# Optimization experiments

Hardware: AMD Instinct MI355X
Metric: run time of the kernel (lower is better)

Reference implementation:

```python
import jax, jax.numpy as jnp
import numpy as np

D, H, DFF, MD = 1024, 16, 4096, 128
B, TS, TT = 8, 512, 512
EPS = 1e-6


def _ln(x, s, b):
    m = jnp.mean(x, axis=-1, keepdims=True)
    v = jnp.mean((x - m) ** 2, axis=-1, keepdims=True)
    return (x - m) * jax.lax.rsqrt(v + EPS) * s + b


def _rel_bias(emb, qlen, klen):
    # T5-style bidirectional bucket: [H, qlen, klen]
    q = jnp.arange(qlen)[:, None]
    k = jnp.arange(klen)[None, :]
    rp = k - q
    bucket = jnp.where(rp < 0, jnp.minimum(-rp, MD - 1), jnp.minimum(rp, MD - 1) + MD)
    return emb[bucket].transpose(2, 0, 1)


def _mha(xq, xkv, w_in, b_in, w_out, b_out, bias):
    # nn.MultiheadAttention math: packed in_proj [3D,D], additive attn bias [H,Tq,Tk]
    Bq, Tq, _ = xq.shape
    Tk = xkv.shape[1]
    hd = D // H
    wq, wk, wv = jnp.split(w_in, 3, axis=0)
    bq, bk, bv = jnp.split(b_in, 3, axis=0)
    q = (xq @ wq.T + bq).reshape(Bq, Tq, H, hd).transpose(0, 2, 1, 3)
    k = (xkv @ wk.T + bk).reshape(Bq, Tk, H, hd).transpose(0, 2, 1, 3)
    v = (xkv @ wv.T + bv).reshape(Bq, Tk, H, hd).transpose(0, 2, 1, 3)
    scores = jnp.einsum('bhqd,bhkd->bhqk', q, k) / jnp.sqrt(jnp.asarray(hd, xq.dtype))
    scores = scores + bias[None]
    attn = jax.nn.softmax(scores, axis=-1)
    out = jnp.einsum('bhqk,bhkd->bhqd', attn, v)
    out = out.transpose(0, 2, 1, 3).reshape(Bq, Tq, D)
    return out @ w_out.T + b_out


def setup_inputs() -> dict:
    key = jax.random.key(0)
    ks = jax.random.split(key, 40)
    std = 0.02

    def n(i, shape):
        return jax.random.normal(ks[i], shape, dtype=jnp.float32) * std

    return {
        'src': jax.random.normal(ks[0], (B, TS, D), dtype=jnp.float32),
        'tgt': jax.random.normal(ks[1], (B, TT, D), dtype=jnp.float32),
        # encoder layer
        'enc_in_w': n(2, (3 * D, D)), 'enc_in_b': jnp.zeros((3 * D,)),
        'enc_out_w': n(3, (D, D)), 'enc_out_b': jnp.zeros((D,)),
        'enc_ff1_w': n(4, (DFF, D)), 'enc_ff1_b': jnp.zeros((DFF,)),
        'enc_ff2_w': n(5, (D, DFF)), 'enc_ff2_b': jnp.zeros((D,)),
        'enc_n1_s': jnp.ones((D,)), 'enc_n1_b': jnp.zeros((D,)),
        'enc_n2_s': jnp.ones((D,)), 'enc_n2_b': jnp.zeros((D,)),
        'enc_rel': n(6, (2 * MD, H)),
        # decoder layer
        'dec_sa_in_w': n(7, (3 * D, D)), 'dec_sa_in_b': jnp.zeros((3 * D,)),
        'dec_sa_out_w': n(8, (D, D)), 'dec_sa_out_b': jnp.zeros((D,)),
        'dec_ca_in_w': n(9, (3 * D, D)), 'dec_ca_in_b': jnp.zeros((3 * D,)),
        'dec_ca_out_w': n(10, (D, D)), 'dec_ca_out_b': jnp.zeros((D,)),
        'dec_ff1_w': n(11, (DFF, D)), 'dec_ff1_b': jnp.zeros((DFF,)),
        'dec_ff2_w': n(12, (D, DFF)), 'dec_ff2_b': jnp.zeros((D,)),
        'dec_n1_s': jnp.ones((D,)), 'dec_n1_b': jnp.zeros((D,)),
        'dec_n2_s': jnp.ones((D,)), 'dec_n2_b': jnp.zeros((D,)),
        'dec_n3_s': jnp.ones((D,)), 'dec_n3_b': jnp.zeros((D,)),
        'dec_rel_self': n(13, (2 * MD, H)),
        'dec_rel_cross': n(14, (2 * MD, H)),
    }


def reference(src, tgt,
              enc_in_w, enc_in_b, enc_out_w, enc_out_b,
              enc_ff1_w, enc_ff1_b, enc_ff2_w, enc_ff2_b,
              enc_n1_s, enc_n1_b, enc_n2_s, enc_n2_b, enc_rel,
              dec_sa_in_w, dec_sa_in_b, dec_sa_out_w, dec_sa_out_b,
              dec_ca_in_w, dec_ca_in_b, dec_ca_out_w, dec_ca_out_b,
              dec_ff1_w, dec_ff1_b, dec_ff2_w, dec_ff2_b,
              dec_n1_s, dec_n1_b, dec_n2_s, dec_n2_b, dec_n3_s, dec_n3_b,
              dec_rel_self, dec_rel_cross):
    Ts, Tt = src.shape[1], tgt.shape[1]

    # ---- encoder layer (pre-LN) ----
    eb = _rel_bias(enc_rel, Ts, Ts)  # [H,Ts,Ts]
    x = src
    x = x + _mha(_ln(x, enc_n1_s, enc_n1_b), _ln(x, enc_n1_s, enc_n1_b),
                 enc_in_w, enc_in_b, enc_out_w, enc_out_b, eb)
    h = _ln(x, enc_n2_s, enc_n2_b)
    x = x + (jax.nn.relu(h @ enc_ff1_w.T + enc_ff1_b) @ enc_ff2_w.T + enc_ff2_b)
    memory = x

    # ---- decoder layer (pre-LN) ----
    causal = jnp.where(jnp.arange(Tt)[None, :] > jnp.arange(Tt)[:, None], -jnp.inf, 0.0)
    sb = _rel_bias(dec_rel_self, Tt, Tt) + causal[None]  # [H,Tt,Tt]
    cb = _rel_bias(dec_rel_cross, Tt, Ts)                # [H,Tt,Ts]
    y = tgt
    yn = _ln(y, dec_n1_s, dec_n1_b)
    y = y + _mha(yn, yn, dec_sa_in_w, dec_sa_in_b, dec_sa_out_w, dec_sa_out_b, sb)
    y = y + _mha(_ln(y, dec_n2_s, dec_n2_b), memory,
                 dec_ca_in_w, dec_ca_in_b, dec_ca_out_w, dec_ca_out_b, cb)
    h = _ln(y, dec_n3_s, dec_n3_b)
    y = y + (jax.nn.relu(h @ dec_ff1_w.T + dec_ff1_b) @ dec_ff2_w.T + dec_ff2_b)
    return y
```

## Files before the change

kernel.cpp:

```cpp
#include <hip/hip_runtime.h>

using u16 = unsigned short;

typedef float f32x4 __attribute__((ext_vector_type(4)));
typedef __bf16 bf16x8v __attribute__((ext_vector_type(8)));
typedef bf16x8v bf16x8 __attribute__((may_alias));
typedef u16 u16x8v __attribute__((ext_vector_type(8)));
typedef u16x8v u16x8 __attribute__((may_alias));
typedef u16 u16x4v __attribute__((ext_vector_type(4)));
typedef u16x4v u16x4 __attribute__((may_alias));
typedef float f32x4v __attribute__((ext_vector_type(4)));
typedef f32x4v float4a __attribute__((may_alias));

#define GPTR(p) ((__attribute__((address_space(1))) void*)(p))
#define LPTR(p) ((__attribute__((address_space(3))) void*)(p))

__device__ __forceinline__ u16 f2bf(float f) {
  unsigned u = __builtin_bit_cast(unsigned, f);
  u += 0x7FFFu + ((u >> 16) & 1u);
  return (u16)(u >> 16);
}

__device__ __forceinline__ f32x4 mfma16(bf16x8 a, bf16x8 b, f32x4 c) {
  return __builtin_amdgcn_mfma_f32_16x16x32_bf16(a, b, c, 0, 0, 0);
}

struct Srcs { const float* s[10]; };

__global__ __launch_bounds__(256) void cvt_all(Srcs srcs, u16* __restrict__ dst) {
  constexpr int off[11] = {0, 786432, 1048576, 2097152, 3145728,
                           3932160, 4194304, 4980736, 5242880, 6291456, 7340032};
  const int i = blockIdx.x * 256 + threadIdx.x;
  int r = 0;
#pragma unroll
  for (int j = 1; j < 10; j++) r += (i >= off[j]);
  float4a v = ((const float4a*)srcs.s[r])[i - off[r]];
  u16x4 o;
  o[0] = f2bf(v[0]); o[1] = f2bf(v[1]); o[2] = f2bf(v[2]); o[3] = f2bf(v[3]);
  ((u16x4*)dst)[i] = o;
}

__global__ __launch_bounds__(256) void add_cvt(const float* __restrict__ a,
                                               const float* __restrict__ b,
                                               u16* __restrict__ o) {
  const int i = blockIdx.x * 256 + threadIdx.x;
  float4a va = ((const float4a*)a)[i];
  float4a vb = ((const float4a*)b)[i];
  u16x4 ov;
#pragma unroll
  for (int j = 0; j < 4; j++) ov[j] = f2bf(va[j] + vb[j]);
  ((u16x4*)o)[i] = ov;
}

__global__ __launch_bounds__(256) void add_f32(float* __restrict__ o,
                                               const float* __restrict__ b) {
  const int i = blockIdx.x * 256 + threadIdx.x;
  float4a vo = ((float4a*)o)[i];
  float4a vb = ((const float4a*)b)[i];
#pragma unroll
  for (int j = 0; j < 4; j++) vo[j] += vb[j];
  ((float4a*)o)[i] = vo;
}

__global__ __launch_bounds__(256) void ln_k(const float* __restrict__ x,
                                            const float* __restrict__ sc,
                                            const float* __restrict__ bi,
                                            u16* __restrict__ out) {
  const int row = blockIdx.x, tid = threadIdx.x;
  float4a v = ((const float4a*)(x + (size_t)row * 1024))[tid];
  float s1 = v[0] + v[1] + v[2] + v[3];
  float s2 = v[0]*v[0] + v[1]*v[1] + v[2]*v[2] + v[3]*v[3];
#pragma unroll
  for (int off = 32; off; off >>= 1) { s1 += __shfl_xor(s1, off); s2 += __shfl_xor(s2, off); }
  __shared__ float red[8];
  if ((tid & 63) == 0) { red[tid >> 6] = s1; red[4 + (tid >> 6)] = s2; }
  __syncthreads();
  s1 = red[0] + red[1] + red[2] + red[3];
  s2 = red[4] + red[5] + red[6] + red[7];
  const float mean = s1 * (1.f / 1024.f);
  const float rstd = rsqrtf(s2 * (1.f / 1024.f) - mean * mean + 1e-6f);
  float4a s4 = ((const float4a*)sc)[tid];
  float4a b4 = ((const float4a*)bi)[tid];
  u16x4 o;
#pragma unroll
  for (int j = 0; j < 4; j++) o[j] = f2bf((v[j] - mean) * rstd * s4[j] + b4[j]);
  ((u16x4*)(out + (size_t)row * 1024))[tid] = o;
}

template <int BN_T, int MW, int EPI, int PF>
__global__ __launch_bounds__(256) void gemm_bt(
    const u16* __restrict__ A, int lda,
    const u16* __restrict__ W, int ldw,
    const float* __restrict__ bias,
    const float* __restrict__ C0, int ldc0,
    void* __restrict__ outv, int ldo, int K,
    float* __restrict__ part) {
  constexpr int BM = 128, BK = 64;
  constexpr int NW = 4 / MW;
  constexpr int FM = BM / MW / 16;
  constexpr int FN = BN_T / NW / 16;
  constexpr int RA = (BM * BK * 2) / 4096;
  constexpr int RB = (BN_T * BK * 2) / 4096;
  constexpr int NB = PF ? 2 : 1;
  __shared__ alignas(16) u16 As[NB][BM * BK];
  __shared__ alignas(16) u16 Bs[NB][BN_T * BK];
  const int tid = threadIdx.x, lane = tid & 63, wv = tid >> 6;
  const int kb = (EPI == 3) ? blockIdx.z * K : 0;

  const int gx = gridDim.x;
  const int nwg = gx * gridDim.y;
  const int orig = blockIdx.y * gx + blockIdx.x;
  const int qq = nwg >> 3, rr = nwg & 7;
  const int xcd = orig & 7, idx = orig >> 3;
  const int wg = (xcd < rr ? xcd * (qq + 1) : rr * (qq + 1) + (xcd - rr) * qq) + idx;
  const int bm = (wg / gx) * BM, bn = (wg % gx) * BN_T;

  const int wr = (wv / NW) * (BM / MW);
  const int wc = (wv % NW) * (BN_T / NW);
  const int la = lane & 15, lg = lane >> 4;
  const int r7 = la & 7;
  const int srow = wv * 8 + (lane >> 3);
  const int scol = ((lane & 7) ^ (lane >> 3)) << 3;
  const u16* gA = A + (size_t)(bm + srow) * lda + scol;
  const u16* gB = W + (size_t)(bn + srow) * ldw + scol;

  f32x4 acc[FM][FN] = {};

  auto stage = [&](int buf, int k0) {
#pragma unroll
    for (int r = 0; r < RA; r++)
      __builtin_amdgcn_global_load_lds(GPTR(gA + (size_t)r * 32 * lda + k0),
                                       LPTR(&As[buf][(wv * 8 + r * 32) * BK]), 16, 0, 0);
#pragma unroll
    for (int r = 0; r < RB; r++)
      __builtin_amdgcn_global_load_lds(GPTR(gB + (size_t)r * 32 * ldw + k0),
                                       LPTR(&Bs[buf][(wv * 8 + r * 32) * BK]), 16, 0, 0);
  };

  auto compute = [&](int buf) {
#pragma unroll
    for (int kk = 0; kk < BK; kk += 32) {
      const int off = ((((kk >> 3) + lg) ^ r7) << 3);
      bf16x8 af[FM], bfr[FN];
#pragma unroll
      for (int m = 0; m < FM; m++)
        af[m] = *(const bf16x8*)&As[buf][(wr + m * 16 + la) * BK + off];
#pragma unroll
      for (int n = 0; n < FN; n++)
        bfr[n] = *(const bf16x8*)&Bs[buf][(wc + n * 16 + la) * BK + off];
#pragma unroll
      for (int m = 0; m < FM; m++)
#pragma unroll
        for (int n = 0; n < FN; n++)
          acc[m][n] = mfma16(af[m], bfr[n], acc[m][n]);
    }
  };

  if constexpr (PF) {
    stage(0, kb);
    int buf = 0;
    const int NT = K / BK;
    for (int t = 0; t < NT; ++t) {
      if (t + 1 < NT) {
        stage(buf ^ 1, kb + (t + 1) * BK);
        if constexpr (RA + RB == 8)
          asm volatile("s_waitcnt vmcnt(8)" ::: "memory");
        else
          asm volatile("s_waitcnt vmcnt(6)" ::: "memory");
      } else {
        asm volatile("s_waitcnt vmcnt(0)" ::: "memory");
      }
      __builtin_amdgcn_s_barrier();
      __builtin_amdgcn_sched_barrier(0);
      compute(buf);
      __builtin_amdgcn_s_barrier();
      buf ^= 1;
    }
  } else {
    for (int k0 = 0; k0 < K; k0 += BK) {
      __syncthreads();
      stage(0, kb + k0);
      __syncthreads();
      compute(0);
    }
  }

  const bool addb = (EPI != 3) || (blockIdx.z == 0);
  float bv[FN];
#pragma unroll
  for (int n = 0; n < FN; n++) bv[n] = addb ? bias[bn + wc + n * 16 + la] : 0.f;
#pragma unroll
  for (int m = 0; m < FM; m++) {
#pragma unroll
    for (int j = 0; j < 4; j++) {
      const int row = bm + wr + m * 16 + (lane >> 4) * 4 + j;
#pragma unroll
      for (int n = 0; n < FN; n++) {
        const int col = bn + wc + n * 16 + la;
        float v = acc[m][n][j] + bv[n];
        if constexpr (EPI == 1) v = fmaxf(v, 0.f);
        if constexpr (EPI == 2) {
          ((float*)outv)[(size_t)row * ldo + col] = v + C0[(size_t)row * ldc0 + col];
        } else if constexpr (EPI == 3) {
          if (blockIdx.z == 0)
            ((float*)outv)[(size_t)row * ldo + col] = v + C0[(size_t)row * ldc0 + col];
          else
            part[(size_t)row * ldo + col] = v;
        } else {
          ((u16*)outv)[(size_t)row * ldo + col] = f2bf(v);
        }
      }
    }
  }
}

template <bool CAUSAL>
__global__ __launch_bounds__(256) void attn_k(
    const u16* __restrict__ Qb, int ldq,
    const u16* __restrict__ Kb, int ldk,
    const u16* __restrict__ Vb, int ldv,
    const float* __restrict__ rel,
    u16* __restrict__ Ob, int ldo,
    int Tq, int Tk) {
  __shared__ alignas(16) u16 Ks[128][72];
  __shared__ alignas(16) u16 Vt[64][136];
  __shared__ alignas(16) u16 Ps[4][16][136];
  __shared__ float biasl[256];
  const int tid = threadIdx.x, lane = tid & 63, w = tid >> 6;
  const int b = blockIdx.y >> 4, h = blockIdx.y & 15;
  const int q0 = blockIdx.x * 64;
  const int la = lane & 15, lg = lane >> 4;

  biasl[tid] = rel[tid * 16 + h];

  const int qr0 = q0 + w * 16;
  const u16* qp = Qb + (size_t)(b * Tq + qr0 + la) * ldq + h * 64 + lg * 8;
  const bf16x8 qf0 = *(const bf16x8*)qp;
  const bf16x8 qf1 = *(const bf16x8*)(qp + 32);

  float m[4], sm[4];
  f32x4 acc[4] = {};
#pragma unroll
  for (int j = 0; j < 4; j++) { m[j] = -1e30f; sm[j] = 0.f; }

  const int kv_end = CAUSAL ? (q0 + 64) : Tk;
  const int srow = tid >> 3, scol = (tid & 7) * 8;
  for (int kv0 = 0; kv0 < kv_end; kv0 += 128) {
    __syncthreads();
#pragma unroll
    for (int r = 0; r < 4; r++) {
      const int row = r * 32 + srow;
      const size_t gr = (size_t)(b * Tk + kv0 + row);
      *(u16x8*)&Ks[row][scol] = *(const u16x8*)&Kb[gr * ldk + h * 64 + scol];
      u16x8 vv = *(const u16x8*)&Vb[gr * ldv + h * 64 + scol];
#pragma unroll
      for (int j = 0; j < 8; j++) Vt[scol + j][row] = vv[j];
    }
    __syncthreads();

    f32x4 s[8];
#pragma unroll
    for (int kvt = 0; kvt < 8; kvt++) {
      const bf16x8 kf0 = *(const bf16x8*)&Ks[kvt * 16 + la][lg * 8];
      const bf16x8 kf1 = *(const bf16x8*)&Ks[kvt * 16 + la][32 + lg * 8];
      f32x4 t = {};
      t = mfma16(qf0, kf0, t);
      t = mfma16(qf1, kf1, t);
      const int kc = kv0 + kvt * 16 + la;
#pragma unroll
      for (int j = 0; j < 4; j++) {
        const int qr = qr0 + lg * 4 + j;
        const int rp = kc - qr;
        const int bucket = rp < 0 ? (rp > -127 ? -rp : 127) : (rp < 127 ? rp : 127) + 128;
        float sv = t[j] * 0.125f + biasl[bucket];
        if (CAUSAL && kc > qr) sv = -1e30f;
        s[kvt][j] = sv;
      }
    }
    float alpha[4];
#pragma unroll
    for (int j = 0; j < 4; j++) {
      float tm = s[0][j];
#pragma unroll
      for (int kvt = 1; kvt < 8; kvt++) tm = fmaxf(tm, s[kvt][j]);
#pragma unroll
      for (int off = 1; off < 16; off <<= 1) tm = fmaxf(tm, __shfl_xor(tm, off));
      const float mn = fmaxf(m[j], tm);
      alpha[j] = __expf(m[j] - mn);
      m[j] = mn;
      float r = 0.f;
#pragma unroll
      for (int kvt = 0; kvt < 8; kvt++) {
        const float p = __expf(s[kvt][j] - mn);
        s[kvt][j] = p;
        r += p;
      }
#pragma unroll
      for (int off = 1; off < 16; off <<= 1) r += __shfl_xor(r, off);
      sm[j] = sm[j] * alpha[j] + r;
    }
#pragma unroll
    for (int kvt = 0; kvt < 8; kvt++)
#pragma unroll
      for (int j = 0; j < 4; j++)
        Ps[w][lg * 4 + j][kvt * 16 + la] = f2bf(s[kvt][j]);
#pragma unroll
    for (int n = 0; n < 4; n++)
#pragma unroll
      for (int j = 0; j < 4; j++)
        acc[n][j] *= alpha[j];
#pragma unroll
    for (int kq = 0; kq < 4; kq++) {
      const bf16x8 pf = *(const bf16x8*)&Ps[w][la][kq * 32 + lg * 8];
#pragma unroll
      for (int n = 0; n < 4; n++) {
        const bf16x8 vf = *(const bf16x8*)&Vt[n * 16 + la][kq * 32 + lg * 8];
        acc[n] = mfma16(pf, vf, acc[n]);
      }
    }
  }
#pragma unroll
  for (int n = 0; n < 4; n++)
#pragma unroll
    for (int j = 0; j < 4; j++) {
      const int qr = qr0 + lg * 4 + j;
      Ob[(size_t)(b * Tq + qr) * ldo + h * 64 + n * 16 + la] = f2bf(acc[n][j] / sm[j]);
    }
}

extern "C" void kernel_launch(void* const* d_in, const int* in_sizes, int n_in,
                              void* d_out, int out_size, void* d_ws, size_t ws_size,
                              hipStream_t stream) {
  (void)in_sizes; (void)n_in; (void)out_size; (void)ws_size;
  const float* src       = (const float*)d_in[0];
  const float* tgt       = (const float*)d_in[1];
  const float* enc_in_w  = (const float*)d_in[2];
  const float* enc_in_b  = (const float*)d_in[3];
  const float* enc_out_w = (const float*)d_in[4];
  const float* enc_out_b = (const float*)d_in[5];
  const float* enc_ff1_w = (const float*)d_in[6];
  const float* enc_ff1_b = (const float*)d_in[7];
  const float* enc_ff2_w = (const float*)d_in[8];
  const float* enc_ff2_b = (const float*)d_in[9];
  const float* enc_n1_s  = (const float*)d_in[10];
  const float* enc_n1_b  = (const float*)d_in[11];
  const float* enc_n2_s  = (const float*)d_in[12];
  const float* enc_n2_b  = (const float*)d_in[13];
  const float* enc_rel   = (const float*)d_in[14];
  const float* dsa_in_w  = (const float*)d_in[15];
  const float* dsa_in_b  = (const float*)d_in[16];
  const float* dsa_out_w = (const float*)d_in[17];
  const float* dsa_out_b = (const float*)d_in[18];
  const float* dca_in_w  = (const float*)d_in[19];
  const float* dca_in_b  = (const float*)d_in[20];
  const float* dca_out_w = (const float*)d_in[21];
  const float* dca_out_b = (const float*)d_in[22];
  const float* dff1_w    = (const float*)d_in[23];
  const float* dff1_b    = (const float*)d_in[24];
  const float* dff2_w    = (const float*)d_in[25];
  const float* dff2_b    = (const float*)d_in[26];
  const float* dn1_s     = (const float*)d_in[27];
  const float* dn1_b     = (const float*)d_in[28];
  const float* dn2_s     = (const float*)d_in[29];
  const float* dn2_b     = (const float*)d_in[30];
  const float* dn3_s     = (const float*)d_in[31];
  const float* dn3_b     = (const float*)d_in[32];
  const float* drel_s    = (const float*)d_in[33];
  const float* drel_c    = (const float*)d_in[34];
  float* fo = (float*)d_out;

  char* w8 = (char*)d_ws;
  float* x_ws  = (float*)(w8 + 0);
  u16* ln_buf  = (u16*)(w8 + 16777216);
  u16* qkv     = (u16*)(w8 + 25165824);
  u16* attn_o  = (u16*)(w8 + 50331648);
  u16* ffh     = qkv;
  u16* memb    = (u16*)(w8 + 58720256);
  u16* wb      = (u16*)(w8 + 67108864);

  u16* w_enc_in  = wb;
  u16* w_enc_out = wb + 3145728;
  u16* w_enc_f1  = wb + 4194304;
  u16* w_enc_f2  = wb + 8388608;
  u16* w_dsa_in  = wb + 12582912;
  u16* w_dsa_out = wb + 15728640;
  u16* w_dca_in  = wb + 16777216;
  u16* w_dca_out = wb + 19922944;
  u16* w_dff1    = wb + 20971520;
  u16* w_dff2    = wb + 25165824;

  Srcs srcs = {{enc_in_w, enc_out_w, enc_ff1_w, enc_ff2_w, dsa_in_w,
                dsa_out_w, dca_in_w, dca_out_w, dff1_w, dff2_w}};
  cvt_all<<<dim3(28672), 256, 0, stream>>>(srcs, wb);

  ln_k<<<dim3(4096), 256, 0, stream>>>(src, enc_n1_s, enc_n1_b, ln_buf);
  gemm_bt<128,2,0,0><<<dim3(24, 32), 256, 0, stream>>>(ln_buf, 1024, w_enc_in, 1024, enc_in_b, nullptr, 0, qkv, 3072, 1024, nullptr);
  attn_k<false><<<dim3(8, 128), 256, 0, stream>>>(qkv, 3072, qkv + 1024, 3072, qkv + 2048, 3072, enc_rel, attn_o, 1024, 512, 512);
  gemm_bt<64,4,2,1><<<dim3(16, 32), 256, 0, stream>>>(attn_o, 1024, w_enc_out, 1024, enc_out_b, src, 1024, x_ws, 1024, 1024, nullptr);
  ln_k<<<dim3(4096), 256, 0, stream>>>(x_ws, enc_n2_s, enc_n2_b, ln_buf);
  gemm_bt<128,2,1,0><<<dim3(32, 32), 256, 0, stream>>>(ln_buf, 1024, w_enc_f1, 1024, enc_ff1_b, nullptr, 0, ffh, 4096, 1024, nullptr);
  gemm_bt<128,2,3,1><<<dim3(8, 32, 2), 256, 0, stream>>>(ffh, 4096, w_enc_f2, 4096, enc_ff2_b, x_ws, 1024, x_ws, 1024, 2048, fo);
  add_cvt<<<dim3(4096), 256, 0, stream>>>(x_ws, fo, memb);

  ln_k<<<dim3(4096), 256, 0, stream>>>(tgt, dn1_s, dn1_b, ln_buf);
  gemm_bt<128,2,0,0><<<dim3(24, 32), 256, 0, stream>>>(ln_buf, 1024, w_dsa_in, 1024, dsa_in_b, nullptr, 0, qkv, 3072, 1024, nullptr);
  attn_k<true><<<dim3(8, 128), 256, 0, stream>>>(qkv, 3072, qkv + 1024, 3072, qkv + 2048, 3072, drel_s, attn_o, 1024, 512, 512);
  gemm_bt<64,4,2,1><<<dim3(16, 32), 256, 0, stream>>>(attn_o, 1024, w_dsa_out, 1024, dsa_out_b, tgt, 1024, fo, 1024, 1024, nullptr);

  ln_k<<<dim3(4096), 256, 0, stream>>>(fo, dn2_s, dn2_b, ln_buf);
  gemm_bt<64,4,0,1><<<dim3(16, 32), 256, 0, stream>>>(ln_buf, 1024, w_dca_in, 1024, dca_in_b, nullptr, 0, qkv, 3072, 1024, nullptr);
  gemm_bt<128,2,0,0><<<dim3(16, 32), 256, 0, stream>>>(memb, 1024, w_dca_in + 1048576, 1024, dca_in_b + 1024, nullptr, 0, qkv + 1024, 3072, 1024, nullptr);
  attn_k<false><<<dim3(8, 128), 256, 0, stream>>>(qkv, 3072, qkv + 1024, 3072, qkv + 2048, 3072, drel_c, attn_o, 1024, 512, 512);
  gemm_bt<64,4,2,1><<<dim3(16, 32), 256, 0, stream>>>(attn_o, 1024, w_dca_out, 1024, dca_out_b, fo, 1024, fo, 1024, 1024, nullptr);

  ln_k<<<dim3(4096), 256, 0, stream>>>(fo, dn3_s, dn3_b, ln_buf);
  gemm_bt<128,2,1,0><<<dim3(32, 32), 256, 0, stream>>>(ln_buf, 1024, w_dff1, 1024, dff1_b, nullptr, 0, ffh, 4096, 1024, nullptr);
  gemm_bt<128,2,3,1><<<dim3(8, 32, 2), 256, 0, stream>>>(ffh, 4096, w_dff2, 4096, dff2_b, fo, 1024, fo, 1024, 2048, x_ws);
  add_f32<<<dim3(4096), 256, 0, stream>>>(fo, x_ws);
}
```

Measured before the change: 613.0 us.

## Prefetch K/V tiles into registers, alias P with K in LDS, swizzle V transpose

The attention kernel now loads the next K/V tile into registers while the current tile's PV matmul runs, hiding global memory latency. The K and P buffers share one LDS region, with an extra barrier between the score phase and the P write, so LDS per block shrinks and occupancy can rise. The transposed V store uses an XOR swizzle on the column index to reduce LDS bank conflicts. In exchange there is an extra __syncthreads per tile and more registers held for the prefetched tiles.

After: 662.2 us. 1.08x slower.

```diff
diff --git a/kernel.cpp b/kernel.cpp
--- a/kernel.cpp
+++ b/kernel.cpp
@@ -222,9 +222,8 @@
     const float* __restrict__ rel,
     u16* __restrict__ Ob, int ldo,
     int Tq, int Tk) {
-  __shared__ alignas(16) u16 Ks[128][72];
+  __shared__ alignas(16) u16 KsPs[128 * 72];
   __shared__ alignas(16) u16 Vt[64][136];
-  __shared__ alignas(16) u16 Ps[4][16][136];
   __shared__ float biasl[256];
   const int tid = threadIdx.x, lane = tid & 63, w = tid >> 6;
   const int b = blockIdx.y >> 4, h = blockIdx.y & 15;
@@ -244,25 +243,35 @@
   for (int j = 0; j < 4; j++) { m[j] = -1e30f; sm[j] = 0.f; }
 
   const int kv_end = CAUSAL ? (q0 + 64) : Tk;
+  const int nt = (kv_end + 127) >> 7;
   const int srow = tid >> 3, scol = (tid & 7) * 8;
-  for (int kv0 = 0; kv0 < kv_end; kv0 += 128) {
+  const int vsw = (tid & 3) * 8;
+  u16* Pw = KsPs + w * 2176;
+
+  u16x8 kreg[4], vreg[4];
+  auto ldtile = [&](int kv0) {
+#pragma unroll
+    for (int r = 0; r < 4; r++) {
+      const size_t gr = (size_t)(b * Tk + kv0 + r * 32 + srow);
+      kreg[r] = *(const u16x8*)&Kb[gr * ldk + h * 64 + scol];
+      vreg[r] = *(const u16x8*)&Vb[gr * ldv + h * 64 + scol];
+    }
+  };
+  ldtile(0);
+
+  for (int ti = 0; ti < nt; ++ti) {
+    const int kv0 = ti << 7;
     __syncthreads();
 #pragma unroll
-    for (int r = 0; r < 4; r++) {
-      const int row = r * 32 + srow;
-      const size_t gr = (size_t)(b * Tk + kv0 + row);
-      *(u16x8*)&Ks[row][scol] = *(const u16x8*)&Kb[gr * ldk + h * 64 + scol];
-      u16x8 vv = *(const u16x8*)&Vb[gr * ldv + h * 64 + scol];
-#pragma unroll
-      for (int j = 0; j < 8; j++) Vt[scol + j][row] = vv[j];
-    }
+    for (int r = 0; r < 4; r++)
+      *(u16x8*)&KsPs[(r * 32 + srow) * 72 + scol] = kreg[r];
     __syncthreads();
 
     f32x4 s[8];
 #pragma unroll
     for (int kvt = 0; kvt < 8; kvt++) {
-      const bf16x8 kf0 = *(const bf16x8*)&Ks[kvt * 16 + la][lg * 8];
-      const bf16x8 kf1 = *(const bf16x8*)&Ks[kvt * 16 + la][32 + lg * 8];
+      const bf16x8 kf0 = *(const bf16x8*)&KsPs[(kvt * 16 + la) * 72 + lg * 8];
+      const bf16x8 kf1 = *(const bf16x8*)&KsPs[(kvt * 16 + la) * 72 + 32 + lg * 8];
       f32x4 t = {};
       t = mfma16(qf0, kf0, t);
       t = mfma16(qf1, kf1, t);
@@ -300,21 +309,34 @@
       sm[j] = sm[j] * alpha[j] + r;
     }
 #pragma unroll
+    for (int r = 0; r < 4; r++) {
+      const int rsw = (r * 32 + srow) ^ vsw;
+#pragma unroll
+      for (int j = 0; j < 8; j++) Vt[scol + j][rsw] = vreg[r][j];
+    }
+    __syncthreads();
+
+#pragma unroll
     for (int kvt = 0; kvt < 8; kvt++)
 #pragma unroll
       for (int j = 0; j < 4; j++)
-        Ps[w][lg * 4 + j][kvt * 16 + la] = f2bf(s[kvt][j]);
+        Pw[(lg * 4 + j) * 136 + kvt * 16 + la] = f2bf(s[kvt][j]);
 #pragma unroll
     for (int n = 0; n < 4; n++)
 #pragma unroll
       for (int j = 0; j < 4; j++)
         acc[n][j] *= alpha[j];
+
+    if (ti + 1 < nt) ldtile(kv0 + 128);
+
 #pragma unroll
     for (int kq = 0; kq < 4; kq++) {
-      const bf16x8 pf = *(const bf16x8*)&Ps[w][la][kq * 32 + lg * 8];
+      const bf16x8 pf = *(const bf16x8*)&Pw[la * 136 + kq * 32 + lg * 8];
 #pragma unroll
       for (int n = 0; n < 4; n++) {
-        const bf16x8 vf = *(const bf16x8*)&Vt[n * 16 + la][kq * 32 + lg * 8];
+        const int dd = n * 16 + la;
+        const int cc = (kq * 32 + lg * 8) ^ (((dd >> 3) & 3) * 8);
+        const bf16x8 vf = *(const bf16x8*)&Vt[dd][cc];
         acc[n] = mfma16(pf, vf, acc[n]);
       }
     }
```

## Split attention KV range across two wave groups with swizzled LDS and merge

Applied to the files above, without the earlier changes.

The attention kernel now launches 512 threads per block as two 4-wave groups, each processing half of the KV tiles with its own K/V LDS buffers. At the end the two partial softmax states are merged through LDS. K tiles are loaded with global_load_lds into an XOR-swizzled layout, and V and P tiles use swizzled indexing to reduce bank conflicts. P now reuses the K buffer, which adds an extra barrier per iteration. The intent is to double parallelism per query tile and cut LDS conflicts, at the cost of more barriers, a merge step and idle groups on short causal ranges.

Result: slower. 1.154 ms (+88.2%).

```diff
diff --git a/kernel.cpp b/kernel.cpp
--- a/kernel.cpp
+++ b/kernel.cpp
@@ -215,25 +215,26 @@
 }
 
 template <bool CAUSAL>
-__global__ __launch_bounds__(256) void attn_k(
+__global__ __launch_bounds__(512, 4) void attn_k(
     const u16* __restrict__ Qb, int ldq,
     const u16* __restrict__ Kb, int ldk,
     const u16* __restrict__ Vb, int ldv,
     const float* __restrict__ rel,
     u16* __restrict__ Ob, int ldo,
     int Tq, int Tk) {
-  __shared__ alignas(16) u16 Ks[128][72];
-  __shared__ alignas(16) u16 Vt[64][136];
-  __shared__ alignas(16) u16 Ps[4][16][136];
+  __shared__ alignas(16) u16 Ks[2][128 * 64];
+  __shared__ alignas(16) u16 Vt[2][64 * 136];
   __shared__ float biasl[256];
   const int tid = threadIdx.x, lane = tid & 63, w = tid >> 6;
+  const int g = w >> 2, ws = w & 3;
+  const int gtid = tid & 255;
   const int b = blockIdx.y >> 4, h = blockIdx.y & 15;
   const int q0 = blockIdx.x * 64;
-  const int la = lane & 15, lg = lane >> 4;
-
-  biasl[tid] = rel[tid * 16 + h];
-
-  const int qr0 = q0 + w * 16;
+  const int la = lane & 15, lg = lane >> 4, r7 = la & 7;
+
+  if (tid < 256) biasl[tid] = rel[tid * 16 + h];
+
+  const int qr0 = q0 + ws * 16;
   const u16* qp = Qb + (size_t)(b * Tq + qr0 + la) * ldq + h * 64 + lg * 8;
   const bf16x8 qf0 = *(const bf16x8*)qp;
   const bf16x8 qf1 = *(const bf16x8*)(qp + 32);
@@ -244,88 +245,144 @@
   for (int j = 0; j < 4; j++) { m[j] = -1e30f; sm[j] = 0.f; }
 
   const int kv_end = CAUSAL ? (q0 + 64) : Tk;
-  const int srow = tid >> 3, scol = (tid & 7) * 8;
-  for (int kv0 = 0; kv0 < kv_end; kv0 += 128) {
+  const int nt = (kv_end + 127) >> 7;
+  const int h0 = (nt + 1) >> 1;
+
+  const int scolK = ((lane & 7) ^ (lane >> 3)) << 3;
+  const u16* gK = Kb + (size_t)(b * Tk + ws * 8 + (lane >> 3)) * ldk + h * 64 + scolK;
+  const int vrow = gtid >> 3;
+  const int vcol = (gtid & 7) * 8;
+  const int vsw = (gtid & 3) * 8;
+  const u16* gV = Vb + (size_t)(b * Tk + vrow) * ldv + h * 64 + vcol;
+  u16* Pw = &Ks[g][ws * 2048];
+
+  for (int i = 0; i < h0; ++i) {
+    const int t = g ? (h0 + i) : i;
+    const bool act = t < nt;
+    const int kv0 = t << 7;
     __syncthreads();
-#pragma unroll
-    for (int r = 0; r < 4; r++) {
-      const int row = r * 32 + srow;
-      const size_t gr = (size_t)(b * Tk + kv0 + row);
-      *(u16x8*)&Ks[row][scol] = *(const u16x8*)&Kb[gr * ldk + h * 64 + scol];
-      u16x8 vv = *(const u16x8*)&Vb[gr * ldv + h * 64 + scol];
-#pragma unroll
-      for (int j = 0; j < 8; j++) Vt[scol + j][row] = vv[j];
+    u16x8 vreg[4];
+    if (act) {
+#pragma unroll
+      for (int r = 0; r < 4; r++)
+        __builtin_amdgcn_global_load_lds(GPTR(gK + (size_t)(kv0 + r * 32) * ldk),
+                                         LPTR(&Ks[g][(ws * 8 + r * 32) * 64]), 16, 0, 0);
+#pragma unroll
+      for (int r = 0; r < 4; r++)
+        vreg[r] = *(const u16x8*)(gV + (size_t)(kv0 + r * 32) * ldv);
     }
     __syncthreads();
-
+    if (act) {
+#pragma unroll
+      for (int r = 0; r < 4; r++) {
+        const int rsw = (r * 32 + vrow) ^ vsw;
+#pragma unroll
+        for (int j = 0; j < 8; j++) Vt[g][(vcol + j) * 136 + rsw] = vreg[r][j];
+      }
+    }
     f32x4 s[8];
-#pragma unroll
-    for (int kvt = 0; kvt < 8; kvt++) {
-      const bf16x8 kf0 = *(const bf16x8*)&Ks[kvt * 16 + la][lg * 8];
-      const bf16x8 kf1 = *(const bf16x8*)&Ks[kvt * 16 + la][32 + lg * 8];
-      f32x4 t = {};
-      t = mfma16(qf0, kf0, t);
-      t = mfma16(qf1, kf1, t);
-      const int kc = kv0 + kvt * 16 + la;
+    float alpha[4];
+    if (act) {
+#pragma unroll
+      for (int kvt = 0; kvt < 8; kvt++) {
+        const bf16x8 kf0 = *(const bf16x8*)&Ks[g][(kvt * 16 + la) * 64 + ((lg ^ r7) << 3)];
+        const bf16x8 kf1 = *(const bf16x8*)&Ks[g][(kvt * 16 + la) * 64 + (((4 + lg) ^ r7) << 3)];
+        f32x4 t2 = {};
+        t2 = mfma16(qf0, kf0, t2);
+        t2 = mfma16(qf1, kf1, t2);
+        const int kc = kv0 + kvt * 16 + la;
+#pragma unroll
+        for (int j = 0; j < 4; j++) {
+          const int qr = qr0 + lg * 4 + j;
+          const int rp = kc - qr;
+          const int bucket = rp < 0 ? (rp > -127 ? -rp : 127) : (rp < 127 ? rp : 127) + 128;
+          float sv = t2[j] * 0.125f + biasl[bucket];
+          if (CAUSAL && kc > qr) sv = -1e30f;
+          s[kvt][j] = sv;
+        }
+      }
 #pragma unroll
       for (int j = 0; j < 4; j++) {
-        const int qr = qr0 + lg * 4 + j;
-        const int rp = kc - qr;
-        const int bucket = rp < 0 ? (rp > -127 ? -rp : 127) : (rp < 127 ? rp : 127) + 128;
-        float sv = t[j] * 0.125f + biasl[bucket];
-        if (CAUSAL && kc > qr) sv = -1e30f;
-        s[kvt][j] = sv;
-      }
-    }
-    float alpha[4];
+        float tm = s[0][j];
+#pragma unroll
+        for (int kvt = 1; kvt < 8; kvt++) tm = fmaxf(tm, s[kvt][j]);
+#pragma unroll
+        for (int off = 1; off < 16; off <<= 1) tm = fmaxf(tm, __shfl_xor(tm, off));
+        const float mn = fmaxf(m[j], tm);
+        alpha[j] = __expf(m[j] - mn);
+        m[j] = mn;
+        float r = 0.f;
+#pragma unroll
+        for (int kvt = 0; kvt < 8; kvt++) {
+          const float p = __expf(s[kvt][j] - mn);
+          s[kvt][j] = p;
+          r += p;
+        }
+#pragma unroll
+        for (int off = 1; off < 16; off <<= 1) r += __shfl_xor(r, off);
+        sm[j] = sm[j] * alpha[j] + r;
+      }
+    }
+    __syncthreads();
+    if (act) {
+#pragma unroll
+      for (int kvt = 0; kvt < 8; kvt++)
+#pragma unroll
+        for (int j = 0; j < 4; j++) {
+          const int row = lg * 4 + j;
+          const int pb = ((kvt * 2 + (la >> 3)) ^ (row & 7)) << 3;
+          Pw[row * 128 + pb + (la & 7)] = f2bf(s[kvt][j]);
+        }
+#pragma unroll
+      for (int n = 0; n < 4; n++)
+#pragma unroll
+        for (int j = 0; j < 4; j++)
+          acc[n][j] *= alpha[j];
+#pragma unroll
+      for (int kq = 0; kq < 4; kq++) {
+        const bf16x8 pf = *(const bf16x8*)&Pw[la * 128 + (((kq * 4 + lg) ^ r7) << 3)];
+#pragma unroll
+        for (int n = 0; n < 4; n++) {
+          const int dd = n * 16 + la;
+          const int cc = (kq * 32 + lg * 8) ^ (((dd >> 3) & 3) * 8);
+          const bf16x8 vf = *(const bf16x8*)&Vt[g][dd * 136 + cc];
+          acc[n] = mfma16(pf, vf, acc[n]);
+        }
+      }
+    }
+  }
+
+  __syncthreads();
+  float* cb = (float*)&Ks[0][0];
+  if (g == 1) {
+    float* p = cb + (ws * 64 + lane) * 24;
+#pragma unroll
+    for (int n = 0; n < 4; n++)
+#pragma unroll
+      for (int j = 0; j < 4; j++) p[n * 4 + j] = acc[n][j];
+#pragma unroll
+    for (int j = 0; j < 4; j++) { p[16 + j] = m[j]; p[20 + j] = sm[j]; }
+  }
+  __syncthreads();
+  if (g == 0) {
+    const float* p = cb + (ws * 64 + lane) * 24;
+    float w0[4], w1[4], inv[4];
 #pragma unroll
     for (int j = 0; j < 4; j++) {
-      float tm = s[0][j];
-#pragma unroll
-      for (int kvt = 1; kvt < 8; kvt++) tm = fmaxf(tm, s[kvt][j]);
-#pragma unroll
-      for (int off = 1; off < 16; off <<= 1) tm = fmaxf(tm, __shfl_xor(tm, off));
-      const float mn = fmaxf(m[j], tm);
-      alpha[j] = __expf(m[j] - mn);
-      m[j] = mn;
-      float r = 0.f;
-#pragma unroll
-      for (int kvt = 0; kvt < 8; kvt++) {
-        const float p = __expf(s[kvt][j] - mn);
-        s[kvt][j] = p;
-        r += p;
-      }
-#pragma unroll
-      for (int off = 1; off < 16; off <<= 1) r += __shfl_xor(r, off);
-      sm[j] = sm[j] * alpha[j] + r;
-    }
-#pragma unroll
-    for (int kvt = 0; kvt < 8; kvt++)
-#pragma unroll
-      for (int j = 0; j < 4; j++)
-        Ps[w][lg * 4 + j][kvt * 16 + la] = f2bf(s[kvt][j]);
+      const float m1 = p[16 + j], s1 = p[20 + j];
+      const float mx = fmaxf(m[j], m1);
+      w0[j] = __expf(m[j] - mx);
+      w1[j] = __expf(m1 - mx);
+      inv[j] = 1.f / (sm[j] * w0[j] + s1 * w1[j]);
+    }
 #pragma unroll
     for (int n = 0; n < 4; n++)
 #pragma unroll
-      for (int j = 0; j < 4; j++)
-        acc[n][j] *= alpha[j];
-#pragma unroll
-    for (int kq = 0; kq < 4; kq++) {
-      const bf16x8 pf = *(const bf16x8*)&Ps[w][la][kq * 32 + lg * 8];
-#pragma unroll
-      for (int n = 0; n < 4; n++) {
-        const bf16x8 vf = *(const bf16x8*)&Vt[n * 16 + la][kq * 32 + lg * 8];
-        acc[n] = mfma16(pf, vf, acc[n]);
-      }
-    }
+      for (int j = 0; j < 4; j++) {
+        const float o = (acc[n][j] * w0[j] + p[n * 4 + j] * w1[j]) * inv[j];
+        Ob[(size_t)(b * Tq + qr0 + lg * 4 + j) * ldo + h * 64 + n * 16 + la] = f2bf(o);
+      }
   }
-#pragma unroll
-  for (int n = 0; n < 4; n++)
-#pragma unroll
-    for (int j = 0; j < 4; j++) {
-      const int qr = qr0 + lg * 4 + j;
-      Ob[(size_t)(b * Tq + qr) * ldo + h * 64 + n * 16 + la] = f2bf(acc[n][j] / sm[j]);
-    }
 }
 
 extern "C" void kernel_launch(void* const* d_in, const int* in_sizes, int n_in,
@@ -395,7 +452,7 @@
 
   ln_k<<<dim3(4096), 256, 0, stream>>>(src, enc_n1_s, enc_n1_b, ln_buf);
   gemm_bt<128,2,0,0><<<dim3(24, 32), 256, 0, stream>>>(ln_buf, 1024, w_enc_in, 1024, enc_in_b, nullptr, 0, qkv, 3072, 1024, nullptr);
-  attn_k<false><<<dim3(8, 128), 256, 0, stream>>>(qkv, 3072, qkv + 1024, 3072, qkv + 2048, 3072, enc_rel, attn_o, 1024, 512, 512);
+  attn_k<false><<<dim3(8, 128), 512, 0, stream>>>(qkv, 3072, qkv + 1024, 3072, qkv + 2048, 3072, enc_rel, attn_o, 1024, 512, 512);
   gemm_bt<64,4,2,1><<<dim3(16, 32), 256, 0, stream>>>(attn_o, 1024, w_enc_out, 1024, enc_out_b, src, 1024, x_ws, 1024, 1024, nullptr);
   ln_k<<<dim3(4096), 256, 0, stream>>>(x_ws, enc_n2_s, enc_n2_b, ln_buf);
   gemm_bt<128,2,1,0><<<dim3(32, 32), 256, 0, stream>>>(ln_buf, 1024, w_enc_f1, 1024, enc_ff1_b, nullptr, 0, ffh, 4096, 1024, nullptr);
@@ -404,13 +461,13 @@
 
   ln_k<<<dim3(4096), 256, 0, stream>>>(tgt, dn1_s, dn1_b, ln_buf);
   gemm_bt<128,2,0,0><<<dim3(24, 32), 256, 0, stream>>>(ln_buf, 1024, w_dsa_in, 1024, dsa_in_b, nullptr, 0, qkv, 3072, 1024, nullptr);
-  attn_k<true><<<dim3(8, 128), 256, 0, stream>>>(qkv, 3072, qkv + 1024, 3072, qkv + 2048, 3072, drel_s, attn_o, 1024, 512, 512);
+  attn_k<true><<<dim3(8, 128), 512, 0, stream>>>(qkv, 3072, qkv + 1024, 3072, qkv + 2048, 3072, drel_s, attn_o, 1024, 512, 512);
   gemm_bt<64,4,2,1><<<dim3(16, 32), 256, 0, stream>>>(attn_o, 1024, w_dsa_out, 1024, dsa_out_b, tgt, 1024, fo, 1024, 1024, nullptr);
 
   ln_k<<<dim3(4096), 256, 0, stream>>>(fo, dn2_s, dn2_b, ln_buf);
   gemm_bt<64,4,0,1><<<dim3(16, 32), 256, 0, stream>>>(ln_buf, 1024, w_dca_in, 1024, dca_in_b, nullptr, 0, qkv, 3072, 1024, nullptr);
   gemm_bt<128,2,0,0><<<dim3(16, 32), 256, 0, stream>>>(memb, 1024, w_dca_in + 1048576, 1024, dca_in_b + 1024, nullptr, 0, qkv + 1024, 3072, 1024, nullptr);
-  attn_k<false><<<dim3(8, 128), 256, 0, stream>>>(qkv, 3072, qkv + 1024, 3072, qkv + 2048, 3072, drel_c, attn_o, 1024, 512, 512);
+  attn_k<false><<<dim3(8, 128), 512, 0, stream>>>(qkv, 3072, qkv + 1024, 3072, qkv + 2048, 3072, drel_c, attn_o, 1024, 512, 512);
   gemm_bt<64,4,2,1><<<dim3(16, 32), 256, 0, stream>>>(attn_o, 1024, w_dca_out, 1024, dca_out_b, fo, 1024, fo, 1024, 1024, nullptr);
 
   ln_k<<<dim3(4096), 256, 0, stream>>>(fo, dn3_s, dn3_b, ln_buf);
```

## Pre-transpose V in a separate kernel and read K/V directly from global in attention

Applied to the files above, without the earlier changes.

A new vt_k kernel transposes each head's V into a [d, Tk] layout in workspace, reusing the x_ws region that is idle at those points. The attention kernel then drops its shared-memory K and V staging and per-tile __syncthreads, and loads K rows and V^T fragments straight from global memory into MFMA operands. The P tile in shared memory gets an XOR swizzle to avoid bank conflicts. The cost is one extra launch and a V round-trip per attention, plus redundant global or L2 reads of K and V across the four waves of a block.

Result: slower. 864.2 us (+41.0%).

```diff
diff --git a/kernel.cpp b/kernel.cpp
--- a/kernel.cpp
+++ b/kernel.cpp
@@ -214,65 +214,82 @@
   }
 }
 
+__global__ __launch_bounds__(256) void vt_k(const u16* __restrict__ V, int ldv,
+                                            u16* __restrict__ vt, int Tk) {
+  __shared__ alignas(16) u16 T[64 * 136];
+  const int tid = threadIdx.x;
+  const int b = blockIdx.y >> 4, h = blockIdx.y & 15;
+  const int kv0 = blockIdx.x * 128;
+  const int srow = tid >> 3, scol = (tid & 7) * 8, vsw = (tid & 3) * 8;
+  const u16* gV = V + (size_t)(b * Tk + kv0 + srow) * ldv + h * 64 + scol;
+#pragma unroll
+  for (int r = 0; r < 4; r++) {
+    u16x8 vv = *(const u16x8*)(gV + (size_t)r * 32 * ldv);
+    const int rsw = (r * 32 + srow) ^ vsw;
+#pragma unroll
+    for (int j = 0; j < 8; j++) T[(scol + j) * 136 + rsw] = vv[j];
+  }
+  __syncthreads();
+  u16* out = vt + (size_t)(blockIdx.y * 64) * 512 + kv0;
+#pragma unroll
+  for (int it = 0; it < 4; it++) {
+    const int task = it * 256 + tid;
+    const int d = task >> 4, c = task & 15;
+    const int cc = (c * 8) ^ (((d >> 3) & 3) * 8);
+    *(u16x8*)(out + (size_t)d * 512 + c * 8) = *(const u16x8*)&T[d * 136 + cc];
+  }
+}
+
 template <bool CAUSAL>
 __global__ __launch_bounds__(256) void attn_k(
     const u16* __restrict__ Qb, int ldq,
     const u16* __restrict__ Kb, int ldk,
-    const u16* __restrict__ Vb, int ldv,
+    const u16* __restrict__ vt,
     const float* __restrict__ rel,
     u16* __restrict__ Ob, int ldo,
     int Tq, int Tk) {
-  __shared__ alignas(16) u16 Ks[128][72];
-  __shared__ alignas(16) u16 Vt[64][136];
-  __shared__ alignas(16) u16 Ps[4][16][136];
+  __shared__ alignas(16) u16 Ps[4][2048];
   __shared__ float biasl[256];
   const int tid = threadIdx.x, lane = tid & 63, w = tid >> 6;
   const int b = blockIdx.y >> 4, h = blockIdx.y & 15;
   const int q0 = blockIdx.x * 64;
-  const int la = lane & 15, lg = lane >> 4;
+  const int la = lane & 15, lg = lane >> 4, r7 = la & 7;
 
   biasl[tid] = rel[tid * 16 + h];
+  __syncthreads();
 
   const int qr0 = q0 + w * 16;
   const u16* qp = Qb + (size_t)(b * Tq + qr0 + la) * ldq + h * 64 + lg * 8;
   const bf16x8 qf0 = *(const bf16x8*)qp;
   const bf16x8 qf1 = *(const bf16x8*)(qp + 32);
 
+  const u16* Kh = Kb + (size_t)(b * Tk) * ldk + h * 64;
+  const u16* Vh = vt + (size_t)(blockIdx.y) * 64 * 512;
+  u16* Pw = Ps[w];
+
   float m[4], sm[4];
   f32x4 acc[4] = {};
 #pragma unroll
   for (int j = 0; j < 4; j++) { m[j] = -1e30f; sm[j] = 0.f; }
 
   const int kv_end = CAUSAL ? (q0 + 64) : Tk;
-  const int srow = tid >> 3, scol = (tid & 7) * 8;
   for (int kv0 = 0; kv0 < kv_end; kv0 += 128) {
-    __syncthreads();
-#pragma unroll
-    for (int r = 0; r < 4; r++) {
-      const int row = r * 32 + srow;
-      const size_t gr = (size_t)(b * Tk + kv0 + row);
-      *(u16x8*)&Ks[row][scol] = *(const u16x8*)&Kb[gr * ldk + h * 64 + scol];
-      u16x8 vv = *(const u16x8*)&Vb[gr * ldv + h * 64 + scol];
-#pragma unroll
-      for (int j = 0; j < 8; j++) Vt[scol + j][row] = vv[j];
-    }
-    __syncthreads();
-
     f32x4 s[8];
 #pragma unroll
     for (int kvt = 0; kvt < 8; kvt++) {
-      const bf16x8 kf0 = *(const bf16x8*)&Ks[kvt * 16 + la][lg * 8];
-      const bf16x8 kf1 = *(const bf16x8*)&Ks[kvt * 16 + la][32 + lg * 8];
-      f32x4 t = {};
-      t = mfma16(qf0, kf0, t);
-      t = mfma16(qf1, kf1, t);
+      const u16* kp = Kh + (size_t)(kv0 + kvt * 16 + la) * ldk + lg * 8;
+      const bf16x8 kf0 = *(const bf16x8*)kp;
+      const bf16x8 kf1 = *(const bf16x8*)(kp + 32);
+      f32x4 t2 = {};
+      t2 = mfma16(qf0, kf0, t2);
+      t2 = mfma16(qf1, kf1, t2);
       const int kc = kv0 + kvt * 16 + la;
 #pragma unroll
       for (int j = 0; j < 4; j++) {
         const int qr = qr0 + lg * 4 + j;
         const int rp = kc - qr;
         const int bucket = rp < 0 ? (rp > -127 ? -rp : 127) : (rp < 127 ? rp : 127) + 128;
-        float sv = t[j] * 0.125f + biasl[bucket];
+        float sv = t2[j] * 0.125f + biasl[bucket];
         if (CAUSAL && kc > qr) sv = -1e30f;
         s[kvt][j] = sv;
       }
@@ -302,8 +319,11 @@
 #pragma unroll
     for (int kvt = 0; kvt < 8; kvt++)
 #pragma unroll
-      for (int j = 0; j < 4; j++)
-        Ps[w][lg * 4 + j][kvt * 16 + la] = f2bf(s[kvt][j]);
+      for (int j = 0; j < 4; j++) {
+        const int row = lg * 4 + j;
+        const int pb = ((kvt * 2 + (la >> 3)) ^ (row & 7)) << 3;
+        Pw[row * 128 + pb + (la & 7)] = f2bf(s[kvt][j]);
+      }
 #pragma unroll
     for (int n = 0; n < 4; n++)
 #pragma unroll
@@ -311,10 +331,11 @@
         acc[n][j] *= alpha[j];
 #pragma unroll
     for (int kq = 0; kq < 4; kq++) {
-      const bf16x8 pf = *(const bf16x8*)&Ps[w][la][kq * 32 + lg * 8];
+      const bf16x8 pf = *(const bf16x8*)&Pw[la * 128 + (((kq * 4 + lg) ^ r7) << 3)];
 #pragma unroll
       for (int n = 0; n < 4; n++) {
-        const bf16x8 vf = *(const bf16x8*)&Vt[n * 16 + la][kq * 32 + lg * 8];
+        const int dd = n * 16 + la;
+        const bf16x8 vf = *(const bf16x8*)&Vh[(size_t)dd * 512 + kv0 + kq * 32 + lg * 8];
         acc[n] = mfma16(pf, vf, acc[n]);
       }
     }
@@ -371,6 +392,7 @@
 
   char* w8 = (char*)d_ws;
   float* x_ws  = (float*)(w8 + 0);
+  u16* vt      = (u16*)(w8 + 0);
   u16* ln_buf  = (u16*)(w8 + 16777216);
   u16* qkv     = (u16*)(w8 + 25165824);
   u16* attn_o  = (u16*)(w8 + 50331648);
@@ -395,7 +417,8 @@
 
   ln_k<<<dim3(4096), 256, 0, stream>>>(src, enc_n1_s, enc_n1_b, ln_buf);
   gemm_bt<128,2,0,0><<<dim3(24, 32), 256, 0, stream>>>(ln_buf, 1024, w_enc_in, 1024, enc_in_b, nullptr, 0, qkv, 3072, 1024, nullptr);
-  attn_k<false><<<dim3(8, 128), 256, 0, stream>>>(qkv, 3072, qkv + 1024, 3072, qkv + 2048, 3072, enc_rel, attn_o, 1024, 512, 512);
+  vt_k<<<dim3(4, 128), 256, 0, stream>>>(qkv + 2048, 3072, vt, 512);
+  attn_k<false><<<dim3(8, 128), 256, 0, stream>>>(qkv, 3072, qkv + 1024, 3072, vt, enc_rel, attn_o, 1024, 512, 512);
   gemm_bt<64,4,2,1><<<dim3(16, 32), 256, 0, stream>>>(attn_o, 1024, w_enc_out, 1024, enc_out_b, src, 1024, x_ws, 1024, 1024, nullptr);
   ln_k<<<dim3(4096), 256, 0, stream>>>(x_ws, enc_n2_s, enc_n2_b, ln_buf);
   gemm_bt<128,2,1,0><<<dim3(32, 32), 256, 0, stream>>>(ln_buf, 1024, w_enc_f1, 1024, enc_ff1_b, nullptr, 0, ffh, 4096, 1024, nullptr);
@@ -404,13 +427,15 @@
 
   ln_k<<<dim3(4096), 256, 0, stream>>>(tgt, dn1_s, dn1_b, ln_buf);
   gemm_bt<128,2,0,0><<<dim3(24, 32), 256, 0, stream>>>(ln_buf, 1024, w_dsa_in, 1024, dsa_in_b, nullptr, 0, qkv, 3072, 1024, nullptr);
-  attn_k<true><<<dim3(8, 128), 256, 0, stream>>>(qkv, 3072, qkv + 1024, 3072, qkv + 2048, 3072, drel_s, attn_o, 1024, 512, 512);
+  vt_k<<<dim3(4, 128), 256, 0, stream>>>(qkv + 2048, 3072, vt, 512);
+  attn_k<true><<<dim3(8, 128), 256, 0, stream>>>(qkv, 3072, qkv + 1024, 3072, vt, drel_s, attn_o, 1024, 512, 512);
   gemm_bt<64,4,2,1><<<dim3(16, 32), 256, 0, stream>>>(attn_o, 1024, w_dsa_out, 1024, dsa_out_b, tgt, 1024, fo, 1024, 1024, nullptr);
 
   ln_k<<<dim3(4096), 256, 0, stream>>>(fo, dn2_s, dn2_b, ln_buf);
   gemm_bt<64,4,0,1><<<dim3(16, 32), 256, 0, stream>>>(ln_buf, 1024, w_dca_in, 1024, dca_in_b, nullptr, 0, qkv, 3072, 1024, nullptr);
   gemm_bt<128,2,0,0><<<dim3(16, 32), 256, 0, stream>>>(memb, 1024, w_dca_in + 1048576, 1024, dca_in_b + 1024, nullptr, 0, qkv + 1024, 3072, 1024, nullptr);
-  attn_k<false><<<dim3(8, 128), 256, 0, stream>>>(qkv, 3072, qkv + 1024, 3072, qkv + 2048, 3072, drel_c, attn_o, 1024, 512, 512);
+  vt_k<<<dim3(4, 128), 256, 0, stream>>>(qkv + 2048, 3072, vt, 512);
+  attn_k<false><<<dim3(8, 128), 256, 0, stream>>>(qkv, 3072, qkv + 1024, 3072, vt, drel_c, attn_o, 1024, 512, 512);
   gemm_bt<64,4,2,1><<<dim3(16, 32), 256, 0, stream>>>(attn_o, 1024, w_dca_out, 1024, dca_out_b, fo, 1024, fo, 1024, 1024, nullptr);
 
   ln_k<<<dim3(4096), 256, 0, stream>>>(fo, dn3_s, dn3_b, ln_buf);
```
